# Optimization experiments

Hardware: AMD Instinct MI355X
Metric: run time of the kernel (lower is better)

Reference implementation:

```python
import jax, jax.numpy as jnp
import numpy as np

N = 50000
E = 800000
IN_C = 128
OUT_C = 64
NEG_SLOPE = 0.2


def setup_inputs() -> dict:
    key = jax.random.key(0)
    k1, k2, k3, k4, k5 = jax.random.split(key, 5)
    x = jax.random.normal(k1, (N, IN_C), dtype=jnp.float32)
    edge_index = jax.random.randint(k2, (2, E), 0, N, dtype=jnp.int64)
    # GATv2Conv params (heads=1): lin_l (source), lin_r (target), att, bias
    sc_in = 1.0 / np.sqrt(IN_C)
    sc_out = 1.0 / np.sqrt(OUT_C)
    W_l = jax.random.normal(k3, (IN_C, OUT_C), dtype=jnp.float32) * sc_in
    W_r = jax.random.normal(k4, (IN_C, OUT_C), dtype=jnp.float32) * sc_in
    att = jax.random.normal(k5, (OUT_C,), dtype=jnp.float32) * sc_out
    bias = jnp.zeros((OUT_C,), dtype=jnp.float32)
    return {"x": x, "edge_index": edge_index, "W_l": W_l, "W_r": W_r,
            "att": att, "bias": bias}


def _gatv2(x, edge_index, W_l, W_r, att, bias):
    n = x.shape[0]
    # add self loops (PyG default add_self_loops=True)
    loop = jnp.arange(n, dtype=edge_index.dtype)
    src = jnp.concatenate([edge_index[0], loop])
    dst = jnpp_concat = jnp.concatenate([edge_index[1], loop])
    x_l = x @ W_l  # source transform [N, C]
    x_r = x @ W_r  # target transform [N, C]
    x_j = x_l[src]                      # [E+N, C] gathered source msgs
    e = jax.nn.leaky_relu(x_j + x_r[dst], NEG_SLOPE)
    logit = e @ att                     # [E+N]
    # segment softmax over edges grouped by destination node
    m = jax.ops.segment_max(logit, dst, num_segments=n)
    m = jnp.where(jnp.isfinite(m), m, 0.0)
    a = jnp.exp(logit - m[dst])
    denom = jax.ops.segment_sum(a, dst, num_segments=n)
    alpha = a / (denom[dst] + 1e-16)
    out = jax.ops.segment_sum(x_j * alpha[:, None], dst, num_segments=n)
    return out + bias


def reference(x, edge_index, W_l, W_r, att, bias):
    # dropout(p=0.6) is identity at inference
    h = jax.nn.elu(_gatv2(x, edge_index, W_l, W_r, att, bias))
    return jax.nn.log_softmax(h, axis=-1)
```

## Files before the change

kernel.cpp:

```cpp
#include <hip/hip_runtime.h>

#define N_NODES 50000
#define N_EDGES 800000
#define E_TOT   (N_EDGES + N_NODES)
#define IN_C    128
#define OUT_C   64
#define NEG_SLOPE 0.2f

#define CAP     64
#define NPART   6250

#define FILL_CHUNK  1024
#define FILL_NCHUNK ((E_TOT + FILL_CHUNK - 1) / FILL_CHUNK)

typedef __bf16 bf16_8 __attribute__((ext_vector_type(8)));
typedef float  f32x4  __attribute__((ext_vector_type(4)));

__device__ __forceinline__ unsigned f2bf(float f) {
    unsigned u = __float_as_uint(f);
    return (u + 0x7fffu + ((u >> 16) & 1u)) >> 16;
}

#define XPAD 136
__global__ __launch_bounds__(256) void k_gemm(
    const float* __restrict__ x, const float* __restrict__ Wl,
    const float* __restrict__ Wr, const float* __restrict__ att,
    unsigned short* __restrict__ xlb, float* __restrict__ xr,
    float* __restrict__ qtil)
{
    __shared__ unsigned short xs[64 * XPAD];
    __shared__ unsigned short wt[128 * XPAD];

    const int tid   = threadIdx.x;
    const int nbase = blockIdx.x * 64;

    const float4* x4 = (const float4*)x;
    for (int i = tid; i < 2048; i += 256) {
        int row = i >> 5, qq = i & 31;
        int node = nbase + row;
        float4 v = make_float4(0.f, 0.f, 0.f, 0.f);
        if (node < N_NODES) v = x4[(size_t)node * 32 + qq];
        uint2 p;
        p.x = f2bf(v.x) | (f2bf(v.y) << 16);
        p.y = f2bf(v.z) | (f2bf(v.w) << 16);
        *(uint2*)&xs[row * XPAD + qq * 4] = p;
    }
    {
        int c = tid >> 1, kh = (tid & 1) * 64;
        const float* Wm = (c < 64) ? Wl : Wr;
        int cm = c & 63;
        for (int kk = 0; kk < 64; kk += 2) {
            float a = Wm[(size_t)(kh + kk) * 64 + cm];
            float b = Wm[(size_t)(kh + kk + 1) * 64 + cm];
            *(unsigned*)&wt[c * XPAD + kh + kk] = f2bf(a) | (f2bf(b) << 16);
        }
    }
    __syncthreads();

    const int lane = tid & 63, wave = tid >> 6;
    const int m = lane & 15, quad = lane >> 4;

    bf16_8 af[4];
#pragma unroll
    for (int kt = 0; kt < 4; ++kt)
        af[kt] = *(const bf16_8*)&xs[(wave * 16 + m) * XPAD + kt * 32 + quad * 8];

    f32x4 accs[4];
#pragma unroll
    for (int t = 0; t < 4; ++t) {
        f32x4 acc = {0.f, 0.f, 0.f, 0.f};
#pragma unroll
        for (int kt = 0; kt < 4; ++kt) {
            bf16_8 bfr = *(const bf16_8*)&wt[(t * 16 + m) * XPAD + kt * 32 + quad * 8];
            acc = __builtin_amdgcn_mfma_f32_16x16x32_bf16(af[kt], bfr, acc, 0, 0, 0);
        }
        accs[t] = acc;
#pragma unroll
        for (int r = 0; r < 4; ++r) {
            int node = nbase + wave * 16 + quad * 4 + r;
            if (node < N_NODES)
                xlb[(size_t)node * 64 + t * 16 + m] = (unsigned short)f2bf(acc[r]);
        }
    }
    {
        float am[4];
#pragma unroll
        for (int t = 0; t < 4; ++t) am[t] = 0.6f * att[t * 16 + m];
        float part[4];
#pragma unroll
        for (int r = 0; r < 4; ++r) {
            part[r] = am[0] * accs[0][r];
#pragma unroll
            for (int t = 1; t < 4; ++t) part[r] = fmaf(am[t], accs[t][r], part[r]);
        }
#pragma unroll
        for (int o = 1; o <= 8; o <<= 1)
#pragma unroll
            for (int r = 0; r < 4; ++r) part[r] += __shfl_xor(part[r], o);
        if (m == 0) {
#pragma unroll
            for (int r = 0; r < 4; ++r) {
                int node = nbase + wave * 16 + quad * 4 + r;
                if (node < N_NODES) qtil[node] = part[r];
            }
        }
    }
#pragma unroll
    for (int t = 4; t < 8; ++t) {
        f32x4 acc = {0.f, 0.f, 0.f, 0.f};
#pragma unroll
        for (int kt = 0; kt < 4; ++kt) {
            bf16_8 bfr = *(const bf16_8*)&wt[(t * 16 + m) * XPAD + kt * 32 + quad * 8];
            acc = __builtin_amdgcn_mfma_f32_16x16x32_bf16(af[kt], bfr, acc, 0, 0, 0);
        }
        int col = t * 16 + m - 64;
#pragma unroll
        for (int r = 0; r < 4; ++r) {
            int node = nbase + wave * 16 + quad * 4 + r;
            if (node < N_NODES) xr[(size_t)node * 64 + col] = acc[r];
        }
    }
}

__global__ __launch_bounds__(256) void k_fill(
    const int* __restrict__ ei, int* __restrict__ cnt, int* __restrict__ csr_src)
{
    int part  = blockIdx.x & 7;
    int chunk = blockIdx.x >> 3;
    int lo = part * NPART, hi = lo + NPART;
#pragma unroll
    for (int i = 0; i < 4; ++i) {
        int e = chunk * FILL_CHUNK + i * 256 + threadIdx.x;
        if (e >= E_TOT) break;
        int dst = (e < N_EDGES) ? ei[N_EDGES + e] : e - N_EDGES;
        if (dst >= lo && dst < hi) {
            int src = (e < N_EDGES) ? ei[e] : dst;
            int pos = atomicAdd(&cnt[dst], 1);
            if (pos < CAP) csr_src[(size_t)dst * CAP + pos] = src;
        }
    }
}

__global__ __launch_bounds__(256) void k_fused(
    const int* __restrict__ cnt, const int* __restrict__ csr_src,
    const unsigned short* __restrict__ xlb, const float* __restrict__ xr,
    const float* __restrict__ qtil, const float* __restrict__ att,
    const float* __restrict__ bias, float* __restrict__ out)
{
    int wid  = (blockIdx.x * 256 + threadIdx.x) >> 6;
    if (wid >= N_NODES) return;
    int lane = threadIdx.x & 63;
    int g = lane >> 3;
    int q = lane & 7;

    const uint4* xl4 = (const uint4*)xlb;
    const int*   cs  = csr_src + (size_t)wid * CAP;

    const float4* xrp = (const float4*)(xr + (size_t)wid * 64 + q * 8);
    float4 xra = xrp[0], xrb = xrp[1];
    const float4* atp = (const float4*)(att + q * 8);
    float4 ata = atp[0], atb = atp[1];
    float xrv[8] = {xra.x, xra.y, xra.z, xra.w, xrb.x, xrb.y, xrb.z, xrb.w};
    float atv[8] = {ata.x, ata.y, ata.z, ata.w, atb.x, atb.y, atb.z, atb.w};
#pragma unroll
    for (int j = 0; j < 8; ++j) atv[j] *= 0.4f;

    int deg = cnt[wid];
    if (deg > CAP) deg = CAP;
    int iters = (deg + 7) >> 3;

    float s = 0.f;
    float acc[8] = {0.f, 0.f, 0.f, 0.f, 0.f, 0.f, 0.f, 0.f};

    int e = g;
    bool va = e < deg;
    int sA = va ? cs[e] : wid;
    uint4 A = xl4[(size_t)sA * 8 + q];
    float QA = qtil[sA];
    e += 8;
    bool vb = e < deg;
    int sB = vb ? cs[e] : wid;
    uint4 B = xl4[(size_t)sB * 8 + q];
    float QB = qtil[sB];

    for (int it = 0; it < iters; ++it) {
        uint4 C = A; float QC = QA; bool vc = va;
        A = B; QA = QB; va = vb;
        e += 8;
        vb = e < deg;
        int sN = vb ? cs[e] : wid;
        B = xl4[(size_t)sN * 8 + q];
        QB = qtil[sN];

        float c[8];
        c[0] = __uint_as_float(C.x << 16);
        c[1] = __uint_as_float(C.x & 0xffff0000u);
        c[2] = __uint_as_float(C.y << 16);
        c[3] = __uint_as_float(C.y & 0xffff0000u);
        c[4] = __uint_as_float(C.z << 16);
        c[5] = __uint_as_float(C.z & 0xffff0000u);
        c[6] = __uint_as_float(C.w << 16);
        c[7] = __uint_as_float(C.w & 0xffff0000u);

        float r = 0.f;
#pragma unroll
        for (int j = 0; j < 8; ++j) {
            float t = c[j] + xrv[j];
            r = fmaf(atv[j], fabsf(t), r);
        }
        r += __shfl_xor(r, 1);
        r += __shfl_xor(r, 2);
        r += __shfl_xor(r, 4);

        float w = vc ? __expf(QC + r) : 0.f;
        s += w;
#pragma unroll
        for (int j = 0; j < 8; ++j) acc[j] = fmaf(w, c[j], acc[j]);
    }

#pragma unroll
    for (int o = 8; o <= 32; o <<= 1) {
        s += __shfl_xor(s, o);
#pragma unroll
        for (int j = 0; j < 8; ++j) acc[j] += __shfl_xor(acc[j], o);
    }

    float inv = 1.f / (s + 1e-16f);
    const float4* bp = (const float4*)(bias + q * 8);
    float4 ba = bp[0], bb = bp[1];
    float bv[8] = {ba.x, ba.y, ba.z, ba.w, bb.x, bb.y, bb.z, bb.w};
    float h[8];
    float mx = -INFINITY;
#pragma unroll
    for (int j = 0; j < 8; ++j) {
        float hh = fmaf(acc[j], inv, bv[j]);
        hh = (hh > 0.f) ? hh : (__expf(hh) - 1.f);
        h[j] = hh;
        mx = fmaxf(mx, hh);
    }
#pragma unroll
    for (int o = 1; o <= 4; o <<= 1) mx = fmaxf(mx, __shfl_xor(mx, o));
    float ex = 0.f;
#pragma unroll
    for (int j = 0; j < 8; ++j) ex += __expf(h[j] - mx);
#pragma unroll
    for (int o = 1; o <= 4; o <<= 1) ex += __shfl_xor(ex, o);
    float lse = mx + __logf(ex);

    if (g == 0) {
        float4* op = (float4*)(out + (size_t)wid * 64 + q * 8);
        op[0] = make_float4(h[0] - lse, h[1] - lse, h[2] - lse, h[3] - lse);
        op[1] = make_float4(h[4] - lse, h[5] - lse, h[6] - lse, h[7] - lse);
    }
}

extern "C" void kernel_launch(void* const* d_in, const int* in_sizes, int n_in,
                              void* d_out, int out_size, void* d_ws, size_t ws_size,
                              hipStream_t stream)
{
    const float* x    = (const float*)d_in[0];
    const int*   ei   = (const int*)  d_in[1];
    const float* Wl   = (const float*)d_in[2];
    const float* Wr   = (const float*)d_in[3];
    const float* att  = (const float*)d_in[4];
    const float* bias = (const float*)d_in[5];
    float* out = (float*)d_out;

    char* w = (char*)d_ws;
    unsigned short* xlb = (unsigned short*)w; w += (size_t)N_NODES * 64 * 2;
    float* xr      = (float*)w;  w += (size_t)N_NODES * 64 * 4;
    int*   csr_src = (int*)w;    w += (size_t)N_NODES * CAP * 4;
    int*   cnt     = (int*)w;    w += (size_t)N_NODES * 4;
    float* qtil    = (float*)w;  w += (size_t)N_NODES * 4;

    hipMemsetAsync(cnt, 0, (size_t)N_NODES * 4, stream);

    k_gemm <<<(N_NODES + 63) / 64,        256, 0, stream>>>(x, Wl, Wr, att, xlb, xr, qtil);
    k_fill <<<FILL_NCHUNK * 8,            256, 0, stream>>>(ei, cnt, csr_src);
    k_fused<<<(N_NODES * 64 + 255) / 256, 256, 0, stream>>>(cnt, csr_src, xlb, xr, qtil, att, bias, out);
}
```

Measured before the change: 167.7 us.

## Merge GEMM and CSR fill kernels into one launch; coalesce weight staging

Combines the projection GEMM and the CSR bucket-fill into a single kernel, using block index ranges to pick which role each block runs. This removes one launch and lets the atomic-heavy fill overlap with the MFMA GEMM blocks on the GPU. It also rewrites the weight-to-LDS transpose to read W with coalesced float2 loads instead of strided column reads. Fill blocks now reserve the GEMM's large LDS allocation, which may limit how many of them are resident at once.

Result: no change. 167.0 us (-0.4%).

```diff
diff --git a/kernel.cpp b/kernel.cpp
--- a/kernel.cpp
+++ b/kernel.cpp
@@ -13,6 +13,9 @@
 #define FILL_CHUNK  1024
 #define FILL_NCHUNK ((E_TOT + FILL_CHUNK - 1) / FILL_CHUNK)
 
+#define G_GEMM  ((N_NODES + 63) / 64)
+#define G_FILL  (FILL_NCHUNK * 8)
+
 typedef __bf16 bf16_8 __attribute__((ext_vector_type(8)));
 typedef float  f32x4  __attribute__((ext_vector_type(4)));
 
@@ -22,16 +25,37 @@
 }
 
 #define XPAD 136
-__global__ __launch_bounds__(256) void k_gemm(
+__global__ __launch_bounds__(256) void k_gemm_fill(
     const float* __restrict__ x, const float* __restrict__ Wl,
     const float* __restrict__ Wr, const float* __restrict__ att,
-    unsigned short* __restrict__ xlb, float* __restrict__ xr,
-    float* __restrict__ qtil)
+    const int* __restrict__ ei, int* __restrict__ cnt,
+    int* __restrict__ csr_src, unsigned short* __restrict__ xlb,
+    float* __restrict__ xr, float* __restrict__ qtil)
 {
     __shared__ unsigned short xs[64 * XPAD];
     __shared__ unsigned short wt[128 * XPAD];
 
-    const int tid   = threadIdx.x;
+    const int tid = threadIdx.x;
+
+    if (blockIdx.x >= G_GEMM) {
+        int bid   = blockIdx.x - G_GEMM;
+        int part  = bid & 7;
+        int chunk = bid >> 3;
+        int lo = part * NPART, hi = lo + NPART;
+#pragma unroll
+        for (int i = 0; i < 4; ++i) {
+            int e = chunk * FILL_CHUNK + i * 256 + tid;
+            if (e >= E_TOT) break;
+            int dst = (e < N_EDGES) ? ei[N_EDGES + e] : e - N_EDGES;
+            if (dst >= lo && dst < hi) {
+                int src = (e < N_EDGES) ? ei[e] : dst;
+                int pos = atomicAdd(&cnt[dst], 1);
+                if (pos < CAP) csr_src[(size_t)dst * CAP + pos] = src;
+            }
+        }
+        return;
+    }
+
     const int nbase = blockIdx.x * 64;
 
     const float4* x4 = (const float4*)x;
@@ -46,13 +70,16 @@
         *(uint2*)&xs[row * XPAD + qq * 4] = p;
     }
     {
-        int c = tid >> 1, kh = (tid & 1) * 64;
-        const float* Wm = (c < 64) ? Wl : Wr;
-        int cm = c & 63;
-        for (int kk = 0; kk < 64; kk += 2) {
-            float a = Wm[(size_t)(kh + kk) * 64 + cm];
-            float b = Wm[(size_t)(kh + kk + 1) * 64 + cm];
-            *(unsigned*)&wt[c * XPAD + kh + kk] = f2bf(a) | (f2bf(b) << 16);
+        const float2* Wl2 = (const float2*)Wl;
+        const float2* Wr2 = (const float2*)Wr;
+        for (int i = tid; i < 8192; i += 256) {
+            int k    = (i >> 5) & 127;
+            int half = i >> 12;
+            int cp   = i & 31;
+            float2 v = half ? Wr2[(size_t)k * 32 + cp] : Wl2[(size_t)k * 32 + cp];
+            int c = half * 64 + cp * 2;
+            wt[c * XPAD + k]       = (unsigned short)f2bf(v.x);
+            wt[(c + 1) * XPAD + k] = (unsigned short)f2bf(v.y);
         }
     }
     __syncthreads();
@@ -118,25 +145,6 @@
         for (int r = 0; r < 4; ++r) {
             int node = nbase + wave * 16 + quad * 4 + r;
             if (node < N_NODES) xr[(size_t)node * 64 + col] = acc[r];
-        }
-    }
-}
-
-__global__ __launch_bounds__(256) void k_fill(
-    const int* __restrict__ ei, int* __restrict__ cnt, int* __restrict__ csr_src)
-{
-    int part  = blockIdx.x & 7;
-    int chunk = blockIdx.x >> 3;
-    int lo = part * NPART, hi = lo + NPART;
-#pragma unroll
-    for (int i = 0; i < 4; ++i) {
-        int e = chunk * FILL_CHUNK + i * 256 + threadIdx.x;
-        if (e >= E_TOT) break;
-        int dst = (e < N_EDGES) ? ei[N_EDGES + e] : e - N_EDGES;
-        if (dst >= lo && dst < hi) {
-            int src = (e < N_EDGES) ? ei[e] : dst;
-            int pos = atomicAdd(&cnt[dst], 1);
-            if (pos < CAP) csr_src[(size_t)dst * CAP + pos] = src;
         }
     }
 }
@@ -275,7 +283,8 @@
 
     hipMemsetAsync(cnt, 0, (size_t)N_NODES * 4, stream);
 
-    k_gemm <<<(N_NODES + 63) / 64,        256, 0, stream>>>(x, Wl, Wr, att, xlb, xr, qtil);
-    k_fill <<<FILL_NCHUNK * 8,            256, 0, stream>>>(ei, cnt, csr_src);
-    k_fused<<<(N_NODES * 64 + 255) / 256, 256, 0, stream>>>(cnt, csr_src, xlb, xr, qtil, att, bias, out);
-}
+    k_gemm_fill<<<G_GEMM + G_FILL,           256, 0, stream>>>(
+        x, Wl, Wr, att, ei, cnt, csr_src, xlb, xr, qtil);
+    k_fused    <<<(N_NODES * 64 + 255) / 256, 256, 0, stream>>>(
+        cnt, csr_src, xlb, xr, qtil, att, bias, out);
+}
```
